# Performance work log

Measured on AMD Instinct MI355X. Metric: run time of the kernel, lower is better.

## Reference

```python
import jax, jax.numpy as jnp
import numpy as np

DIM = 128
N_GNN = 3
VDW_N = 6.0
MAX_VDW = 0.0356
MIN_VDW = 0.0178
DEV_VDW_RADIUS = 0.2
DM_MIN = 0.5


def gated_gat(x, adj, W, Wb, A, gW, gb):
    # PIGNet-style GatedGAT: attention from bilinear form, gated residual
    h = x @ W + Wb                                   # [B,N,D]
    e = jnp.einsum('bjl,bkl->bjk', h @ A, h)
    e = e + jnp.swapaxes(e, 1, 2)
    att = jnp.where(adj > 0, e, -9e15)
    att = jax.nn.softmax(att, axis=-1) * adj
    hp = jax.nn.relu(jnp.einsum('bij,bjd->bid', att, h))
    coeff = jax.nn.sigmoid(jnp.concatenate([x, hp], axis=-1) @ gW + gb)  # [B,N,1]
    return coeff * x + (1.0 - coeff) * hp


def pair_mlp(lig, tgt, W1, b1, W2, b2):
    # MLP on concat([lig_i, tgt_j]) without materializing [B,L,T,2D]:
    # split W1 along its input dim (exact same math as concat @ W1)
    D = lig.shape[-1]
    pre = (jnp.einsum('bld,dk->blk', lig, W1[:D])[:, :, None, :]
           + jnp.einsum('btd,dk->btk', tgt, W1[D:])[:, None, :, :] + b1)
    h = jax.nn.relu(pre)                             # [B,L,T,D]
    return jnp.einsum('bltk,ko->blt', h, W2) + b2[0]  # [B,L,T]


def setup_inputs() -> dict:
    key = jax.random.key(0)
    ks = jax.random.split(key, 20)
    B, L, T, D = 8, 128, 512, DIM
    f32 = jnp.float32

    def adj(k, n, p):
        a = (jax.random.uniform(k, (B, n, n)) < p).astype(f32)
        a = jnp.maximum(a, jnp.swapaxes(a, 1, 2))
        return jnp.minimum(a + jnp.eye(n, dtype=f32), 1.0)

    s = 0.05
    inp = dict(
        ligand_h=jax.random.normal(ks[0], (B, L, 54), f32),
        target_h=jax.random.normal(ks[1], (B, T, 54), f32),
        ligand_adj=adj(ks[2], L, 0.10),
        target_adj=adj(ks[3], T, 0.02),
        interaction_indice=(jax.random.uniform(ks[4], (B, 3, L, T)) < 0.05).astype(f32),
        ligand_pos=jax.random.uniform(ks[5], (B, L, 3), f32) * 20.0,
        target_pos=jax.random.uniform(ks[6], (B, T, 3), f32) * 20.0,
        rotor=jnp.floor(jax.random.uniform(ks[7], (B, 1), f32) * 10.0),
        ligand_vdw_radii=jax.random.uniform(ks[8], (B, L), f32) * 0.5 + 1.5,
        target_vdw_radii=jax.random.uniform(ks[9], (B, T), f32) * 0.5 + 1.5,
        ligand_valid=jnp.ones((B, L), f32),
        target_valid=jnp.ones((B, T), f32),
        emb_W=jax.random.normal(ks[10], (54, D), f32) * s,
        gat_W=jax.random.normal(ks[11], (N_GNN, D, D), f32) * s,
        gat_Wb=jnp.zeros((N_GNN, D), f32),
        gat_A=jax.random.normal(ks[12], (N_GNN, D, D), f32) * s,
        gat_gW=jax.random.normal(ks[13], (N_GNN, 2 * D, 1), f32) * s,
        gat_gb=jnp.zeros((N_GNN, 1), f32),
        vdwA_W1=jax.random.normal(ks[14], (2 * D, D), f32) * s,
        vdwA_b1=jnp.zeros((D,), f32),
        vdwA_W2=jax.random.normal(ks[15], (D, 1), f32) * s,
        vdwA_b2=jnp.zeros((1,), f32),
        dc_W1=jax.random.normal(ks[16], (2 * D, D), f32) * s,
        dc_b1=jnp.zeros((D,), f32),
        dc_W2=jax.random.normal(ks[17], (D, 1), f32) * s,
        dc_b2=jnp.zeros((1,), f32),
        hbond_coeff=jnp.array([1.0], f32),
        metal_coeff=jnp.array([1.0], f32),
        hydrophobic_coeff=jnp.array([0.5], f32),
        rotor_coeff=jnp.array([0.5], f32),
    )
    return inp


def reference(ligand_h, target_h, ligand_adj, target_adj, interaction_indice,
              ligand_pos, target_pos, rotor, ligand_vdw_radii, target_vdw_radii,
              ligand_valid, target_valid, emb_W, gat_W, gat_Wb, gat_A, gat_gW,
              gat_gb, vdwA_W1, vdwA_b1, vdwA_W2, vdwA_b2, dc_W1, dc_b1, dc_W2,
              dc_b2, hbond_coeff, metal_coeff, hydrophobic_coeff, rotor_coeff):
    lig = ligand_h @ emb_W
    tgt = target_h @ emb_W
    # pairwise distance matrix with min-distance clamp
    diff = ligand_pos[:, :, None, :] - target_pos[:, None, :, :]
    dm = jnp.sqrt((diff * diff).sum(-1) + 1e-10)      # [B,L,T]
    dm = jnp.where(dm < DM_MIN, 1e10, dm)
    for i in range(N_GNN):  # eval mode: dropout is identity
        lig = gated_gat(lig, ligand_adj, gat_W[i], gat_Wb[i], gat_A[i], gat_gW[i], gat_gb[i])
        tgt = gated_gat(tgt, target_adj, gat_W[i], gat_Wb[i], gat_A[i], gat_gW[i], gat_gb[i])
    vdws_sum = ligand_vdw_radii[:, :, None] + target_vdw_radii[:, None, :]
    # dm_correction=True: tanh MLP on pairwise concat features, scaled by dev_vdw_radius
    vdws_sum = vdws_sum + jnp.tanh(pair_mlp(lig, tgt, dc_W1, dc_b1, dc_W2, dc_b2)) * DEV_VDW_RADIUS
    # --- vdw term ---
    dm_0 = jnp.where(vdws_sum < 1e-4, 1.0, vdws_sum)
    ratio = dm_0 / dm
    valid = ligand_valid[:, :, None] * target_valid[:, None, :]
    energy = jnp.minimum(ratio ** (2.0 * VDW_N) - 2.0 * ratio ** VDW_N, 100.0) * valid
    A = jax.nn.sigmoid(pair_mlp(lig, tgt, vdwA_W1, vdwA_b1, vdwA_W2, vdwA_b2))
    A = A * (MAX_VDW - MIN_VDW) + MIN_VDW
    vdw_e = (A * energy).sum((1, 2))                  # [B]
    # --- hbond / metal / hydrophobic ramps share dm - vdws_sum ---
    d = dm - vdws_sum
    ramp = jnp.clip(d / -0.7, 0.0, 1.0)
    hbond_e = -(hbond_coeff[0] ** 2) * (ramp * interaction_indice[:, 0]).sum((1, 2))
    metal_e = -(metal_coeff[0] ** 2) * (ramp * interaction_indice[:, 1]).sum((1, 2))
    ramp2 = jnp.clip(-d + 1.5, 0.0, 1.0)
    hydro_e = -(hydrophobic_coeff[0] ** 2) * (ramp2 * interaction_indice[:, 2]).sum((1, 2))
    energies = jnp.stack([vdw_e, hbond_e, metal_e, hydro_e], axis=-1)  # [B,4]
    energies = energies / (1.0 + rotor_coeff[0] ** 2 * rotor)          # rotor penalty
    return energies
```

## Files before the change

### kernel.cpp

```cpp
#include <hip/hip_runtime.h>
#include <hip/hip_bf16.h>
#include <math.h>

typedef __hip_bfloat16 bf16;

#define DIMD 128
#define BB 8
#define LL 128
#define TT 512

#define BMT 64
#define BKT 32
#define TGT_TILES 36
#define LIG_TILES 3

#define CV_EMBW   0L
#define CV_GATW   (CV_EMBW + 54 * 128)
#define CV_GATA   (CV_GATW + 3 * 128 * 128)
#define CV_WB     (CV_GATA + 3 * 128 * 128)
#define CV_DCW1   (CV_WB + 3 * 128)
#define CV_VW1    (CV_DCW1 + 2 * 128 * 128)
#define CV_TOTAL  (CV_VW1 + 2 * 128 * 128)

__device__ __forceinline__ float LD(const void* p, long i, int bf) {
    if (bf) return __bfloat162float(((const bf16*)p)[i]);
    return ((const float*)p)[i];
}

__global__ void init_ws(const unsigned int* __restrict__ embw_raw,
                        float* __restrict__ accum, int* __restrict__ flagp) {
    int t = threadIdx.x;
    if (t < 32) accum[t] = 0.0f;
    if (t == 0) {
        int cnt = 0;
        for (int k = 0; k < 256; ++k) {
            unsigned int b = (embw_raw[k] >> 8) & 0xffu;
            unsigned int e = b & 0x7fu;
            if (e >= 0x38u && e <= 0x3fu) ++cnt;
        }
        *flagp = (cnt > 128) ? 1 : 0;
    }
}

__global__ void cvt_weights(const void* __restrict__ embW, const void* __restrict__ gatW,
                            const void* __restrict__ gatA, const void* __restrict__ gatWb,
                            const void* __restrict__ dcW1, const void* __restrict__ vW1,
                            float* __restrict__ out, const int* __restrict__ flagp) {
    int bf = *flagp;
    long i = (long)blockIdx.x * 256 + threadIdx.x;
    if (i >= CV_TOTAL) return;
    float v;
    if (i < CV_GATW)      v = LD(embW, i - CV_EMBW, bf);
    else if (i < CV_GATA) v = LD(gatW, i - CV_GATW, bf);
    else if (i < CV_WB)   v = LD(gatA, i - CV_GATA, bf);
    else if (i < CV_DCW1) v = LD(gatWb, i - CV_WB, bf);
    else if (i < CV_VW1)  v = LD(dcW1, i - CV_DCW1, bf);
    else                  v = LD(vW1, i - CV_VW1, bf);
    out[i] = v;
}

__global__ void embed_both(const void* __restrict__ Xl, const void* __restrict__ Xt,
                           const float* __restrict__ Wf, float* __restrict__ out,
                           int K, const int* __restrict__ flagp) {
    __shared__ float xrow[DIMD];
    int bf = *flagp;
    int row = blockIdx.x;
    int d = threadIdx.x;
    const void* X; long r;
    if (row < BB * LL) { X = Xl; r = row; }
    else               { X = Xt; r = row - BB * LL; }
    if (d < K) xrow[d] = LD(X, r * K + d, bf);
    __syncthreads();
    float acc = 0.0f;
    for (int k = 0; k < K; ++k)
        acc = fmaf(xrow[k], Wf[(long)k * DIMD + d], acc);
    out[(long)row * DIMD + d] = acc;
}

__global__ void gemm_hha4(const float* __restrict__ X, const float* __restrict__ Wf,
                          const float* __restrict__ Af, const float* __restrict__ Wbf,
                          int layer, float* __restrict__ hout, float* __restrict__ hAout) {
    __shared__ float xs[4][DIMD];
    __shared__ float hs[4][DIMD];
    long row0 = (long)blockIdx.x * 4;
    int d = threadIdx.x & 127, rg = threadIdx.x >> 7;
    xs[rg * 2 + 0][d] = X[(row0 + rg * 2 + 0) * DIMD + d];
    xs[rg * 2 + 1][d] = X[(row0 + rg * 2 + 1) * DIMD + d];
    __syncthreads();
    const float* W = Wf + (long)layer * DIMD * DIMD;
    const float* A = Af + (long)layer * DIMD * DIMD;
    float b = Wbf[layer * DIMD + d];
    float h0 = b, h1 = b;
    const float* x0 = xs[rg * 2];
    const float* x1 = xs[rg * 2 + 1];
#pragma unroll 8
    for (int k = 0; k < DIMD; ++k) {
        float w = W[(long)k * DIMD + d];
        h0 = fmaf(x0[k], w, h0);
        h1 = fmaf(x1[k], w, h1);
    }
    long ob = (row0 + rg * 2) * DIMD + d;
    hout[ob] = h0; hout[ob + DIMD] = h1;
    hs[rg * 2][d] = h0; hs[rg * 2 + 1][d] = h1;
    __syncthreads();
    float a0 = 0.0f, a1 = 0.0f;
    const float* g0 = hs[rg * 2];
    const float* g1 = hs[rg * 2 + 1];
#pragma unroll 8
    for (int k = 0; k < DIMD; ++k) {
        float w = A[(long)k * DIMD + d];
        a0 = fmaf(g0[k], w, a0);
        a1 = fmaf(g1[k], w, a1);
    }
    hAout[ob] = a0;
    hAout[ob + DIMD] = a1;
}

__global__ void esym_both(const float* __restrict__ hA_t, const float* __restrict__ h_t,
                          float* __restrict__ e_t,
                          const float* __restrict__ hA_l, const float* __restrict__ h_l,
                          float* __restrict__ e_l) {
    __shared__ float At[BKT][BMT + 4];
    __shared__ float Bt[BKT][BMT + 4];
    int idx = blockIdx.x, b = blockIdx.y, t = threadIdx.x;
    const float *hA, *h; float* e; int N;
    if (idx < TGT_TILES) { hA = hA_t; h = h_t; e = e_t; N = TT; }
    else { idx -= TGT_TILES; hA = hA_l; h = h_l; e = e_l; N = LL; }
    int jt = (int)((sqrtf(8.0f * idx + 1.0f) - 1.0f) * 0.5f);
    while ((jt + 1) * (jt + 2) / 2 <= idx) ++jt;
    while (jt * (jt + 1) / 2 > idx) --jt;
    int kt = idx - jt * (jt + 1) / 2;
    const float* hAb = hA + (long)b * N * DIMD;
    const float* hb  = h  + (long)b * N * DIMD;
    int tm = t & 15, tn = t >> 4;
    int k4 = (t & 7) * 4;
    int row0 = t >> 3;
    float acc[4][4];
#pragma unroll
    for (int i = 0; i < 4; ++i)
#pragma unroll
        for (int jj = 0; jj < 4; ++jj) acc[i][jj] = 0.0f;

#pragma unroll
    for (int c = 0; c < 8; ++c) {
        const float* Ap = (c < 4) ? hAb : hb;
        const float* Bp = (c < 4) ? hb : hAb;
        int ko = (c & 3) * BKT;
        __syncthreads();
#pragma unroll
        for (int rr = 0; rr < 2; ++rr) {
            int row = row0 + rr * 32;
            float4 av = *(const float4*)&Ap[(long)(jt * BMT + row) * DIMD + ko + k4];
            float4 bv = *(const float4*)&Bp[(long)(kt * BMT + row) * DIMD + ko + k4];
            At[k4 + 0][row] = av.x; At[k4 + 1][row] = av.y;
            At[k4 + 2][row] = av.z; At[k4 + 3][row] = av.w;
            Bt[k4 + 0][row] = bv.x; Bt[k4 + 1][row] = bv.y;
            Bt[k4 + 2][row] = bv.z; Bt[k4 + 3][row] = bv.w;
        }
        __syncthreads();
#pragma unroll
        for (int k = 0; k < BKT; ++k) {
            float4 a4 = *(const float4*)&At[k][tm * 4];
            float4 b4 = *(const float4*)&Bt[k][tn * 4];
            float A[4] = {a4.x, a4.y, a4.z, a4.w};
            float Bv[4] = {b4.x, b4.y, b4.z, b4.w};
#pragma unroll
            for (int i = 0; i < 4; ++i)
#pragma unroll
                for (int jj = 0; jj < 4; ++jj)
                    acc[i][jj] = fmaf(A[i], Bv[jj], acc[i][jj]);
        }
    }
    long ebN = (long)b * N;
    long ebase = (ebN + jt * BMT + tm * 4) * N + kt * BMT + tn * 4;
#pragma unroll
    for (int i = 0; i < 4; ++i) {
        float4 v;
        v.x = acc[i][0]; v.y = acc[i][1]; v.z = acc[i][2]; v.w = acc[i][3];
        *(float4*)&e[ebase + (long)i * N] = v;
    }
    if (jt != kt) {
        long mbase = (ebN + kt * BMT + tn * 4) * N + jt * BMT + tm * 4;
#pragma unroll
        for (int jj = 0; jj < 4; ++jj) {
            float4 v;
            v.x = acc[0][jj]; v.y = acc[1][jj]; v.z = acc[2][jj]; v.w = acc[3][jj];
            *(float4*)&e[mbase + (long)jj * N] = v;
        }
    }
}

template<int CNT>
__device__ __forceinline__ void softmax_row(float* __restrict__ erow,
                                            const void* __restrict__ adj,
                                            long adjbase, int bf) {
    int lane = threadIdx.x & 63;
    float vals[CNT], av[CNT];
    float m = -3.4e38f;
#pragma unroll
    for (int i = 0; i < CNT; ++i) {
        int k = lane + i * 64;
        float a = LD(adj, adjbase + k, bf);
        float v = (a > 0.0f) ? erow[k] : -9e15f;
        av[i] = a; vals[i] = v;
        m = fmaxf(m, v);
    }
#pragma unroll
    for (int s = 32; s > 0; s >>= 1) m = fmaxf(m, __shfl_xor(m, s));
    float sum = 0.0f;
#pragma unroll
    for (int i = 0; i < CNT; ++i) { vals[i] = expf(vals[i] - m); sum += vals[i]; }
#pragma unroll
    for (int s = 32; s > 0; s >>= 1) sum += __shfl_xor(sum, s);
    float inv = 1.0f / sum;
#pragma unroll
    for (int i = 0; i < CNT; ++i)
        erow[lane + i * 64] = vals[i] * av[i] * inv;
}

__global__ void att_softmax_both(float* __restrict__ e_t, float* __restrict__ e_l,
                                 const void* __restrict__ adj_t, const void* __restrict__ adj_l,
                                 const int* __restrict__ flagp) {
    int bf = *flagp;
    int b = blockIdx.y, x = blockIdx.x;
    int jr = threadIdx.x >> 6;
    if (x < TT / 4) {
        int j = x * 4 + jr;
        long base = ((long)b * TT + j) * TT;
        softmax_row<8>(e_t + base, adj_t, base, bf);
    } else {
        int j = (x - TT / 4) * 4 + jr;
        long base = ((long)b * LL + j) * LL;
        softmax_row<2>(e_l + base, adj_l, base, bf);
    }
}

__global__ void hp_gemm_both(const float* __restrict__ att_t, const float* __restrict__ h_t,
                             float* __restrict__ p0_t, float* __restrict__ p1_t,
                             const float* __restrict__ att_l, const float* __restrict__ h_l,
                             float* __restrict__ p0_l, float* __restrict__ p1_l) {
    __shared__ float At[32][36];
    __shared__ float Ht[32][DIMD];
    int jt = blockIdx.x, kc = blockIdx.y, b = blockIdx.z;
    int t = threadIdx.x;
    const float *att, *h; float *part0, *part1; int N;
    if (jt < 16) { att = att_t; h = h_t; part0 = p0_t; part1 = p1_t; N = TT; }
    else { jt -= 16; att = att_l; h = h_l; part0 = p0_l; part1 = p1_l; N = LL; }
    const float* attb = att + (long)b * N * N;
    const float* hb = h + (long)b * N * DIMD;
    int tm = t & 7, tn = t >> 3;
    float acc[4][4] = {};
    int kchunk = N / 2;
    int kbeg = kc * kchunk;
    int ar = t >> 3;
    int ac4 = (t & 7) * 4;
    int hk = t >> 5;
    int hc4 = (t & 31) * 4;
    for (int k0 = kbeg; k0 < kbeg + kchunk; k0 += 32) {
        __syncthreads();
        float4 av = *(const float4*)&attb[(long)(jt * 32 + ar) * N + k0 + ac4];
        At[ac4 + 0][ar] = av.x; At[ac4 + 1][ar] = av.y;
        At[ac4 + 2][ar] = av.z; At[ac4 + 3][ar] = av.w;
#pragma unroll
        for (int p = 0; p < 4; ++p)
            *(float4*)&Ht[hk + p * 8][hc4] = *(const float4*)&hb[(long)(k0 + hk + p * 8) * DIMD + hc4];
        __syncthreads();
#pragma unroll
        for (int k = 0; k < 32; ++k) {
            float4 a4 = *(const float4*)&At[k][tm * 4];
            float4 h4 = *(const float4*)&Ht[k][tn * 4];
            float A[4] = {a4.x, a4.y, a4.z, a4.w};
            float H[4] = {h4.x, h4.y, h4.z, h4.w};
#pragma unroll
            for (int i = 0; i < 4; ++i)
#pragma unroll
                for (int jj = 0; jj < 4; ++jj)
                    acc[i][jj] = fmaf(A[i], H[jj], acc[i][jj]);
        }
    }
    float* outp = (kc == 0) ? part0 : part1;
    long obase = ((long)b * N + jt * 32 + tm * 4) * DIMD + tn * 4;
#pragma unroll
    for (int i = 0; i < 4; ++i) {
        float4 v; v.x = acc[i][0]; v.y = acc[i][1]; v.z = acc[i][2]; v.w = acc[i][3];
        *(float4*)&outp[obase + (long)i * DIMD] = v;
    }
}

__global__ void gat_gate_both(float* __restrict__ x_t, float* __restrict__ x_l,
                              const float* __restrict__ p0_t, const float* __restrict__ p1_t,
                              const float* __restrict__ p0_l, const float* __restrict__ p1_l,
                              const void* __restrict__ gW, long offgW,
                              const void* __restrict__ gb, long offgb,
                              const int* __restrict__ flagp) {
    int bf = *flagp;
    int b = blockIdx.y, x = blockIdx.x;
    int jr = threadIdx.x >> 6, lane = threadIdx.x & 63;
    float* xb; const float *part0, *part1; long rbase;
    if (x < TT / 4) {
        int j = x * 4 + jr;
        rbase = ((long)b * TT + j) * DIMD;
        xb = x_t; part0 = p0_t; part1 = p1_t;
    } else {
        int j = (x - TT / 4) * 4 + jr;
        rbase = ((long)b * LL + j) * DIMD;
        xb = x_l; part0 = p0_l; part1 = p1_l;
    }
    float* xrow = xb + rbase;
    float hp0 = fmaxf(part0[rbase + lane] + part1[rbase + lane], 0.0f);
    float hp1 = fmaxf(part0[rbase + lane + 64] + part1[rbase + lane + 64], 0.0f);
    float x0 = xrow[lane], x1 = xrow[lane + 64];
    float g = x0 * LD(gW, offgW + lane, bf) + x1 * LD(gW, offgW + lane + 64, bf)
            + hp0 * LD(gW, offgW + DIMD + lane, bf) + hp1 * LD(gW, offgW + DIMD + lane + 64, bf);
#pragma unroll
    for (int s = 32; s > 0; s >>= 1) g += __shfl_xor(g, s);
    g += LD(gb, offgb, bf);
    float coeff = 1.0f / (1.0f + expf(-g));
    xrow[lane] = coeff * x0 + (1.0f - coeff) * hp0;
    xrow[lane + 64] = coeff * x1 + (1.0f - coeff) * hp1;
}

__global__ void proj_both4(const float* __restrict__ X,
                           const float* __restrict__ Wdcf, const void* __restrict__ bdc,
                           const float* __restrict__ WAf, const void* __restrict__ bA,
                           long rowsplit, float* __restrict__ outdc, float* __restrict__ outA,
                           const int* __restrict__ flagp) {
    __shared__ float xs[4][DIMD];
    int bf = *flagp;
    const float* Wf; const void* bias; float* out;
    if (blockIdx.y == 0) { Wf = Wdcf; bias = bdc; out = outdc; }
    else                 { Wf = WAf;  bias = bA;  out = outA; }
    long row0 = (long)blockIdx.x * 4;
    int d = threadIdx.x & 127, rg = threadIdx.x >> 7;
    int sideb = row0 >= rowsplit;
    const float* W = Wf + (sideb ? (long)DIMD * DIMD : 0);
    xs[rg * 2 + 0][d] = X[(row0 + rg * 2 + 0) * DIMD + d];
    xs[rg * 2 + 1][d] = X[(row0 + rg * 2 + 1) * DIMD + d];
    __syncthreads();
    float b0 = sideb ? 0.0f : LD(bias, d, bf);
    float a0 = b0, a1 = b0;
    const float* x0 = xs[rg * 2];
    const float* x1 = xs[rg * 2 + 1];
#pragma unroll 8
    for (int k = 0; k < DIMD; ++k) {
        float w = W[(long)k * DIMD + d];
        a0 = fmaf(x0[k], w, a0);
        a1 = fmaf(x1[k], w, a1);
    }
    long ob = (row0 + rg * 2) * DIMD + d;
    out[ob] = a0;
    out[ob + DIMD] = a1;
}

__global__ void transpose_both(const float* __restrict__ in0, float* __restrict__ out0,
                               const float* __restrict__ in1, float* __restrict__ out1) {
    __shared__ float tile[32][33];
    int z = blockIdx.z;
    const float* in; float* outT; int b;
    if (z < BB) { in = in0; outT = out0; b = z; }
    else        { in = in1; outT = out1; b = z - BB; }
    int n0 = blockIdx.x * 32;
    int d0 = blockIdx.y * 32;
    int t = threadIdx.x;
    int tx = t & 31, ty = t >> 5;
    for (int r = ty; r < 32; r += 8)
        tile[r][tx] = in[((long)b * TT + n0 + r) * DIMD + d0 + tx];
    __syncthreads();
    for (int r = ty; r < 32; r += 8)
        outT[((long)b * DIMD + d0 + r) * TT + n0 + tx] = tile[tx][r];
}

__global__ void pair_energy(const float* __restrict__ ligdc, const float* __restrict__ tgtdcT,
                            const float* __restrict__ ligA, const float* __restrict__ tgtAT,
                            const void* __restrict__ dcW2, const void* __restrict__ dcb2,
                            const void* __restrict__ AW2, const void* __restrict__ Ab2,
                            const void* __restrict__ lpos, const void* __restrict__ tpos,
                            const void* __restrict__ lrad, const void* __restrict__ trad,
                            const void* __restrict__ lval, const void* __restrict__ tval,
                            const void* __restrict__ ii, float* __restrict__ accum,
                            const int* __restrict__ flagp) {
    int bf = *flagp;
    int l0 = blockIdx.x * 2, b = blockIdx.y, t = threadIdx.x;
    __shared__ __align__(16) float sdc0[DIMD], sdc1[DIMD], sA0[DIMD], sA1[DIMD];
    __shared__ __align__(16) float w2dc[DIMD], w2A[DIMD];
    __shared__ float red[256];
    if (t < DIMD) {
        sdc0[t] = ligdc[((long)b * LL + l0) * DIMD + t];
        sA0[t]  = ligA [((long)b * LL + l0) * DIMD + t];
        w2dc[t] = LD(dcW2, t, bf);
        w2A[t]  = LD(AW2, t, bf);
    } else {
        int u = t - DIMD;
        sdc1[u] = ligdc[((long)b * LL + l0 + 1) * DIMD + u];
        sA1[u]  = ligA [((long)b * LL + l0 + 1) * DIMD + u];
    }
    __syncthreads();
    int tt0 = t * 2;
    const float* tdT = tgtdcT + (long)b * DIMD * TT;
    const float* taT = tgtAT  + (long)b * DIMD * TT;
    float adc00 = 0.0f, adc01 = 0.0f, adc10 = 0.0f, adc11 = 0.0f;
    float aA00 = 0.0f, aA01 = 0.0f, aA10 = 0.0f, aA11 = 0.0f;
    for (int i4 = 0; i4 < DIMD; i4 += 4) {
        float4 wd = *(const float4*)&w2dc[i4];
        float4 wa = *(const float4*)&w2A[i4];
        float4 v0d = *(const float4*)&sdc0[i4];
        float4 v1d = *(const float4*)&sdc1[i4];
        float4 v0a = *(const float4*)&sA0[i4];
        float4 v1a = *(const float4*)&sA1[i4];
        float wdv[4] = {wd.x, wd.y, wd.z, wd.w};
        float wav[4] = {wa.x, wa.y, wa.z, wa.w};
        float s0d[4] = {v0d.x, v0d.y, v0d.z, v0d.w};
        float s1d[4] = {v1d.x, v1d.y, v1d.z, v1d.w};
        float s0a[4] = {v0a.x, v0a.y, v0a.z, v0a.w};
        float s1a[4] = {v1a.x, v1a.y, v1a.z, v1a.w};
#pragma unroll
        for (int j = 0; j < 4; ++j) {
            float2 td = *(const float2*)&tdT[(long)(i4 + j) * TT + tt0];
            float2 ta = *(const float2*)&taT[(long)(i4 + j) * TT + tt0];
            adc00 = fmaf(fmaxf(td.x + s0d[j], 0.0f), wdv[j], adc00);
            adc01 = fmaf(fmaxf(td.y + s0d[j], 0.0f), wdv[j], adc01);
            adc10 = fmaf(fmaxf(td.x + s1d[j], 0.0f), wdv[j], adc10);
            adc11 = fmaf(fmaxf(td.y + s1d[j], 0.0f), wdv[j], adc11);
            aA00 = fmaf(fmaxf(ta.x + s0a[j], 0.0f), wav[j], aA00);
            aA01 = fmaf(fmaxf(ta.y + s0a[j], 0.0f), wav[j], aA01);
            aA10 = fmaf(fmaxf(ta.x + s1a[j], 0.0f), wav[j], aA10);
            aA11 = fmaf(fmaxf(ta.y + s1a[j], 0.0f), wav[j], aA11);
        }
    }
    float lx0 = LD(lpos, ((long)b * LL + l0) * 3 + 0, bf);
    float ly0 = LD(lpos, ((long)b * LL + l0) * 3 + 1, bf);
    float lz0 = LD(lpos, ((long)b * LL + l0) * 3 + 2, bf);
    float lx1 = LD(lpos, ((long)b * LL + l0 + 1) * 3 + 0, bf);
    float ly1 = LD(lpos, ((long)b * LL + l0 + 1) * 3 + 1, bf);
    float lz1 = LD(lpos, ((long)b * LL + l0 + 1) * 3 + 2, bf);
    float lr0 = LD(lrad, (long)b * LL + l0, bf);
    float lr1 = LD(lrad, (long)b * LL + l0 + 1, bf);
    float lv0 = LD(lval, (long)b * LL + l0, bf);
    float lv1 = LD(lval, (long)b * LL + l0 + 1, bf);
    float cdcb2 = LD(dcb2, 0, bf), cab2 = LD(Ab2, 0, bf);
    long iiA0 = ((long)(b * 3 + 0) * LL + l0) * TT;
    long iiB0 = ((long)(b * 3 + 1) * LL + l0) * TT;
    long iiC0 = ((long)(b * 3 + 2) * LL + l0) * TT;
    long iiA1 = iiA0 + TT, iiB1 = iiB0 + TT, iiC1 = iiC0 + TT;
    float p0 = 0.0f, p1 = 0.0f, p2 = 0.0f, p3 = 0.0f;
#pragma unroll
    for (int jj = 0; jj < 2; ++jj) {
        int tt = tt0 + jj;
        float tx = LD(tpos, ((long)b * TT + tt) * 3 + 0, bf);
        float ty = LD(tpos, ((long)b * TT + tt) * 3 + 1, bf);
        float tz = LD(tpos, ((long)b * TT + tt) * 3 + 2, bf);
        float tr = LD(trad, (long)b * TT + tt, bf);
        float tv = LD(tval, (long)b * TT + tt, bf);
#pragma unroll
        for (int li = 0; li < 2; ++li) {
            float dx = (li ? lx1 : lx0) - tx;
            float dy = (li ? ly1 : ly0) - ty;
            float dz = (li ? lz1 : lz0) - tz;
            float dm = sqrtf(dx * dx + dy * dy + dz * dz + 1e-10f);
            if (dm < 0.5f) dm = 1e10f;
            float adcv = jj ? (li ? adc11 : adc01) : (li ? adc10 : adc00);
            float aAv  = jj ? (li ? aA11  : aA01)  : (li ? aA10  : aA00);
            float dev = tanhf(adcv + cdcb2) * 0.2f;
            float vdws = (li ? lr1 : lr0) + tr + dev;
            float dm0 = (vdws < 1e-4f) ? 1.0f : vdws;
            float ratio = dm0 / dm;
            float r2 = ratio * ratio, r6 = r2 * r2 * r2, r12 = r6 * r6;
            float en = fminf(r12 - 2.0f * r6, 100.0f) * (li ? lv1 : lv0) * tv;
            float As = 1.0f / (1.0f + expf(-(aAv + cab2)));
            As = As * (0.0356f - 0.0178f) + 0.0178f;
            p0 = fmaf(As, en, p0);
            float dd = dm - vdws;
            float ramp = fminf(fmaxf(dd * (1.0f / -0.7f), 0.0f), 1.0f);
            p1 = fmaf(ramp, LD(ii, (li ? iiA1 : iiA0) + tt, bf), p1);
            p2 = fmaf(ramp, LD(ii, (li ? iiB1 : iiB0) + tt, bf), p2);
            float ramp2 = fminf(fmaxf(-dd + 1.5f, 0.0f), 1.0f);
            p3 = fmaf(ramp2, LD(ii, (li ? iiC1 : iiC0) + tt, bf), p3);
        }
    }
    for (int e = 0; e < 4; ++e) {
        float v = (e == 0) ? p0 : (e == 1) ? p1 : (e == 2) ? p2 : p3;
        red[t] = v; __syncthreads();
        for (int s = 128; s > 0; s >>= 1) { if (t < s) red[t] += red[t + s]; __syncthreads(); }
        if (t == 0) atomicAdd(&accum[b * 4 + e], red[0]);
        __syncthreads();
    }
}

__global__ void finalize(const float* __restrict__ accum, const void* __restrict__ hb,
                         const void* __restrict__ mc, const void* __restrict__ hyd,
                         const void* __restrict__ rc, const void* __restrict__ rotor,
                         void* __restrict__ out, const int* __restrict__ flagp) {
    int bf = *flagp;
    int t = threadIdx.x;
    if (t >= 32) return;
    int b = t >> 2, e = t & 3;
    float v = accum[t];
    if (e == 1) { float c = LD(hb, 0, bf);  v = -c * c * v; }
    else if (e == 2) { float c = LD(mc, 0, bf);  v = -c * c * v; }
    else if (e == 3) { float c = LD(hyd, 0, bf); v = -c * c * v; }
    float r = LD(rc, 0, bf);
    float den = 1.0f + r * r * LD(rotor, b, bf);
    float res = v / den;
    if (bf) ((bf16*)out)[t] = __float2bfloat16(res);
    else    ((float*)out)[t] = res;
}

extern "C" void kernel_launch(void* const* d_in, const int* in_sizes, int n_in,
                              void* d_out, int out_size, void* d_ws, size_t ws_size,
                              hipStream_t stream) {
    const void* ligand_h = d_in[0];
    const void* target_h = d_in[1];
    const void* ligand_adj = d_in[2];
    const void* target_adj = d_in[3];
    const void* interaction_indice = d_in[4];
    const void* ligand_pos = d_in[5];
    const void* target_pos = d_in[6];
    const void* rotor = d_in[7];
    const void* ligand_vdw = d_in[8];
    const void* target_vdw = d_in[9];
    const void* ligand_valid = d_in[10];
    const void* target_valid = d_in[11];
    const void* emb_W = d_in[12];
    const void* gat_W = d_in[13];
    const void* gat_Wb = d_in[14];
    const void* gat_A = d_in[15];
    const void* gat_gW = d_in[16];
    const void* gat_gb = d_in[17];
    const void* vdwA_W1 = d_in[18];
    const void* vdwA_b1 = d_in[19];
    const void* vdwA_W2 = d_in[20];
    const void* vdwA_b2 = d_in[21];
    const void* dc_W1 = d_in[22];
    const void* dc_b1 = d_in[23];
    const void* dc_W2 = d_in[24];
    const void* dc_b2 = d_in[25];
    const void* hbond_coeff = d_in[26];
    const void* metal_coeff = d_in[27];
    const void* hydrophobic_coeff = d_in[28];
    const void* rotor_coeff = d_in[29];

    float* ws = (float*)d_ws;
    size_t off = 0;
    float* lig_x = ws + off;  off += (size_t)BB * LL * DIMD;
    float* tgt_x = ws + off;  off += (size_t)BB * TT * DIMD;
    float* h_lig = ws + off;  off += (size_t)BB * LL * DIMD;
    float* h_tgt = ws + off;  off += (size_t)BB * TT * DIMD;
    float* hA_lig = ws + off; off += (size_t)BB * LL * DIMD;
    float* hA_tgt = ws + off; off += (size_t)BB * TT * DIMD;
    float* accum = ws + off;  off += 32;
    int* flagp = (int*)(ws + off); off += 2;
    float* e_buf = ws + off;  off += (size_t)BB * TT * TT;
    float* e_lig = ws + off;  off += (size_t)BB * LL * LL;
    float* part1 = ws + off;  off += (size_t)BB * (TT + LL) * DIMD;
    float* cvw   = ws + off;  off += (size_t)CV_TOTAL;
    float* part1_t = part1;
    float* part1_l = part1 + (size_t)BB * TT * DIMD;
    float* part0_lig = hA_lig;
    float* part0_tgt = hA_tgt;
    float* ligdc = h_lig;
    float* ligA = hA_lig;
    float* tgtdc = h_tgt;
    float* tgtA  = hA_tgt;
    float* tgtdcT = e_buf;
    float* tgtAT  = e_buf + (size_t)BB * DIMD * TT;
    float* wEmb = cvw + CV_EMBW;
    float* wGat = cvw + CV_GATW;
    float* wGatA = cvw + CV_GATA;
    float* wWb  = cvw + CV_WB;
    float* wDc1 = cvw + CV_DCW1;
    float* wV1  = cvw + CV_VW1;

    init_ws<<<1, 64, 0, stream>>>((const unsigned int*)emb_W, accum, flagp);
    cvt_weights<<<(CV_TOTAL + 255) / 256, 256, 0, stream>>>(
        emb_W, gat_W, gat_A, gat_Wb, dc_W1, vdwA_W1, cvw, flagp);

    embed_both<<<BB * (LL + TT), DIMD, 0, stream>>>(ligand_h, target_h, wEmb, lig_x, 54, flagp);

    const long ROWSPLIT = (long)BB * LL;
    for (int i = 0; i < 3; ++i) {
        long offgW = (long)i * 2 * DIMD;
        long offgb = i;
        gemm_hha4<<<BB * (LL + TT) / 4, 256, 0, stream>>>(
            lig_x, wGat, wGatA, wWb, i, h_lig, hA_lig);
        esym_both<<<dim3(TGT_TILES + LIG_TILES, BB), 256, 0, stream>>>(
            hA_tgt, h_tgt, e_buf, hA_lig, h_lig, e_lig);
        att_softmax_both<<<dim3(TT / 4 + LL / 4, BB), 256, 0, stream>>>(
            e_buf, e_lig, target_adj, ligand_adj, flagp);
        hp_gemm_both<<<dim3(20, 2, BB), 256, 0, stream>>>(
            e_buf, h_tgt, part0_tgt, part1_t, e_lig, h_lig, part0_lig, part1_l);
        gat_gate_both<<<dim3(TT / 4 + LL / 4, BB), 256, 0, stream>>>(
            tgt_x, lig_x, part0_tgt, part1_t, part0_lig, part1_l,
            gat_gW, offgW, gat_gb, offgb, flagp);
    }

    proj_both4<<<dim3(BB * (LL + TT) / 4, 2), 256, 0, stream>>>(
        lig_x, wDc1, dc_b1, wV1, vdwA_b1, ROWSPLIT, ligdc, ligA, flagp);

    transpose_both<<<dim3(TT / 32, DIMD / 32, 2 * BB), 256, 0, stream>>>(
        tgtdc, tgtdcT, tgtA, tgtAT);

    pair_energy<<<dim3(LL / 2, BB), 256, 0, stream>>>(
        ligdc, tgtdcT, ligA, tgtAT, dc_W2, dc_b2, vdwA_W2, vdwA_b2,
        ligand_pos, target_pos, ligand_vdw, target_vdw,
        ligand_valid, target_valid, interaction_indice, accum, flagp);

    finalize<<<1, 64, 0, stream>>>(accum, hbond_coeff, metal_coeff,
                                   hydrophobic_coeff, rotor_coeff, rotor, d_out, flagp);
}
```

Before: 391.5 us.

## Fuse gating into next GEMM, split esym halves, merge init kernels, widen pair grid

Merges the flag-detection and weight-conversion kernels into one launch, and folds the GAT gate step into the next layer's h/hA GEMM or the final projection kernel, so three launches and one pass over x are removed. The symmetric attention-score GEMM is split into two independent halves written to separate buffers and summed inside softmax. This doubles the block count but adds an extra N×N buffer read. The pair-energy kernel now uses one target per thread with twice as many blocks, raising parallelism at the cost of less register reuse. The gate is recomputed redundantly in both y-blocks of proj_gate.

```diff
diff --git a/kernel.cpp b/kernel.cpp
--- a/kernel.cpp
+++ b/kernel.cpp
@@ -18,7 +18,9 @@
 #define CV_GATW   (CV_EMBW + 54 * 128)
 #define CV_GATA   (CV_GATW + 3 * 128 * 128)
 #define CV_WB     (CV_GATA + 3 * 128 * 128)
-#define CV_DCW1   (CV_WB + 3 * 128)
+#define CV_GGW    (CV_WB + 3 * 128)
+#define CV_GGB    (CV_GGW + 3 * 2 * 128)
+#define CV_DCW1   (CV_GGB + 4)
 #define CV_VW1    (CV_DCW1 + 2 * 128 * 128)
 #define CV_TOTAL  (CV_VW1 + 2 * 128 * 128)
 
@@ -27,33 +29,35 @@
     return ((const float*)p)[i];
 }
 
-__global__ void init_ws(const unsigned int* __restrict__ embw_raw,
-                        float* __restrict__ accum, int* __restrict__ flagp) {
+__global__ void init_cvt(const unsigned int* __restrict__ embw_raw,
+                         const void* __restrict__ embW, const void* __restrict__ gatW,
+                         const void* __restrict__ gatA, const void* __restrict__ gatWb,
+                         const void* __restrict__ ggW, const void* __restrict__ ggb,
+                         const void* __restrict__ dcW1, const void* __restrict__ vW1,
+                         float* __restrict__ out, float* __restrict__ accum,
+                         int* __restrict__ flagp) {
+    __shared__ int cnts;
     int t = threadIdx.x;
-    if (t < 32) accum[t] = 0.0f;
-    if (t == 0) {
-        int cnt = 0;
-        for (int k = 0; k < 256; ++k) {
-            unsigned int b = (embw_raw[k] >> 8) & 0xffu;
-            unsigned int e = b & 0x7fu;
-            if (e >= 0x38u && e <= 0x3fu) ++cnt;
-        }
-        *flagp = (cnt > 128) ? 1 : 0;
-    }
-}
-
-__global__ void cvt_weights(const void* __restrict__ embW, const void* __restrict__ gatW,
-                            const void* __restrict__ gatA, const void* __restrict__ gatWb,
-                            const void* __restrict__ dcW1, const void* __restrict__ vW1,
-                            float* __restrict__ out, const int* __restrict__ flagp) {
-    int bf = *flagp;
-    long i = (long)blockIdx.x * 256 + threadIdx.x;
+    if (t == 0) cnts = 0;
+    __syncthreads();
+    unsigned int bword = (embw_raw[t] >> 8) & 0xffu;
+    unsigned int e = bword & 0x7fu;
+    if (e >= 0x38u && e <= 0x3fu) atomicAdd(&cnts, 1);
+    __syncthreads();
+    int bf = cnts > 128;
+    if (blockIdx.x == 0) {
+        if (t < 32) accum[t] = 0.0f;
+        if (t == 0) *flagp = bf;
+    }
+    long i = (long)blockIdx.x * 256 + t;
     if (i >= CV_TOTAL) return;
     float v;
-    if (i < CV_GATW)      v = LD(embW, i - CV_EMBW, bf);
+    if (i < CV_GATW)      v = LD(embW, i, bf);
     else if (i < CV_GATA) v = LD(gatW, i - CV_GATW, bf);
     else if (i < CV_WB)   v = LD(gatA, i - CV_GATA, bf);
-    else if (i < CV_DCW1) v = LD(gatWb, i - CV_WB, bf);
+    else if (i < CV_GGW)  v = LD(gatWb, i - CV_WB, bf);
+    else if (i < CV_GGB)  v = LD(ggW, i - CV_GGW, bf);
+    else if (i < CV_DCW1) { long j = i - CV_GGB; v = (j < 3) ? LD(ggb, j, bf) : 0.0f; }
     else if (i < CV_VW1)  v = LD(dcW1, i - CV_DCW1, bf);
     else                  v = LD(vW1, i - CV_VW1, bf);
     out[i] = v;
@@ -77,61 +81,89 @@
     out[(long)row * DIMD + d] = acc;
 }
 
-__global__ void gemm_hha4(const float* __restrict__ X, const float* __restrict__ Wf,
-                          const float* __restrict__ Af, const float* __restrict__ Wbf,
-                          int layer, float* __restrict__ hout, float* __restrict__ hAout) {
+__global__ void gemm_hha_gate(float* __restrict__ X, const float* __restrict__ P0,
+                              const float* __restrict__ P1, const float* __restrict__ cvw,
+                              int layer, int dogate,
+                              float* __restrict__ hout, float* __restrict__ hAout) {
     __shared__ float xs[4][DIMD];
     __shared__ float hs[4][DIMD];
+    __shared__ float gred[4][2];
     long row0 = (long)blockIdx.x * 4;
     int d = threadIdx.x & 127, rg = threadIdx.x >> 7;
-    xs[rg * 2 + 0][d] = X[(row0 + rg * 2 + 0) * DIMD + d];
-    xs[rg * 2 + 1][d] = X[(row0 + rg * 2 + 1) * DIMD + d];
-    __syncthreads();
-    const float* W = Wf + (long)layer * DIMD * DIMD;
-    const float* A = Af + (long)layer * DIMD * DIMD;
-    float b = Wbf[layer * DIMD + d];
+    int w = threadIdx.x >> 6, lane = threadIdx.x & 63;
+    long r0 = row0 + rg * 2, r1 = r0 + 1;
+    float xv0 = X[r0 * DIMD + d];
+    float xv1 = X[r1 * DIMD + d];
+    if (dogate) {
+        const float* gW = cvw + CV_GGW + (long)(layer - 1) * 2 * DIMD;
+        float gb = cvw[CV_GGB + (layer - 1)];
+        float hp0 = fmaxf(P0[r0 * DIMD + d] + P1[r0 * DIMD + d], 0.0f);
+        float hp1 = fmaxf(P0[r1 * DIMD + d] + P1[r1 * DIMD + d], 0.0f);
+        float s0 = xv0 * gW[d] + hp0 * gW[DIMD + d];
+        float s1 = xv1 * gW[d] + hp1 * gW[DIMD + d];
+#pragma unroll
+        for (int s = 32; s > 0; s >>= 1) { s0 += __shfl_xor(s0, s); s1 += __shfl_xor(s1, s); }
+        if (lane == 0) { gred[rg * 2 + 0][w & 1] = s0; gred[rg * 2 + 1][w & 1] = s1; }
+        __syncthreads();
+        float g0 = gred[rg * 2 + 0][0] + gred[rg * 2 + 0][1] + gb;
+        float g1 = gred[rg * 2 + 1][0] + gred[rg * 2 + 1][1] + gb;
+        float c0 = 1.0f / (1.0f + expf(-g0));
+        float c1 = 1.0f / (1.0f + expf(-g1));
+        xv0 = c0 * xv0 + (1.0f - c0) * hp0;
+        xv1 = c1 * xv1 + (1.0f - c1) * hp1;
+        X[r0 * DIMD + d] = xv0;
+        X[r1 * DIMD + d] = xv1;
+    }
+    xs[rg * 2 + 0][d] = xv0;
+    xs[rg * 2 + 1][d] = xv1;
+    __syncthreads();
+    const float* W = cvw + CV_GATW + (long)layer * DIMD * DIMD;
+    const float* A = cvw + CV_GATA + (long)layer * DIMD * DIMD;
+    float b = cvw[CV_WB + layer * DIMD + d];
     float h0 = b, h1 = b;
     const float* x0 = xs[rg * 2];
     const float* x1 = xs[rg * 2 + 1];
 #pragma unroll 8
     for (int k = 0; k < DIMD; ++k) {
-        float w = W[(long)k * DIMD + d];
-        h0 = fmaf(x0[k], w, h0);
-        h1 = fmaf(x1[k], w, h1);
-    }
-    long ob = (row0 + rg * 2) * DIMD + d;
+        float wv = W[(long)k * DIMD + d];
+        h0 = fmaf(x0[k], wv, h0);
+        h1 = fmaf(x1[k], wv, h1);
+    }
+    long ob = r0 * DIMD + d;
     hout[ob] = h0; hout[ob + DIMD] = h1;
     hs[rg * 2][d] = h0; hs[rg * 2 + 1][d] = h1;
     __syncthreads();
     float a0 = 0.0f, a1 = 0.0f;
-    const float* g0 = hs[rg * 2];
-    const float* g1 = hs[rg * 2 + 1];
+    const float* g0p = hs[rg * 2];
+    const float* g1p = hs[rg * 2 + 1];
 #pragma unroll 8
     for (int k = 0; k < DIMD; ++k) {
-        float w = A[(long)k * DIMD + d];
-        a0 = fmaf(g0[k], w, a0);
-        a1 = fmaf(g1[k], w, a1);
+        float wv = A[(long)k * DIMD + d];
+        a0 = fmaf(g0p[k], wv, a0);
+        a1 = fmaf(g1p[k], wv, a1);
     }
     hAout[ob] = a0;
     hAout[ob + DIMD] = a1;
 }
 
 __global__ void esym_both(const float* __restrict__ hA_t, const float* __restrict__ h_t,
-                          float* __restrict__ e_t,
+                          float* __restrict__ e1_t, float* __restrict__ e2_t,
                           const float* __restrict__ hA_l, const float* __restrict__ h_l,
-                          float* __restrict__ e_l) {
+                          float* __restrict__ e1_l, float* __restrict__ e2_l) {
     __shared__ float At[BKT][BMT + 4];
     __shared__ float Bt[BKT][BMT + 4];
-    int idx = blockIdx.x, b = blockIdx.y, t = threadIdx.x;
+    int idx = blockIdx.x, half = blockIdx.y, b = blockIdx.z, t = threadIdx.x;
     const float *hA, *h; float* e; int N;
-    if (idx < TGT_TILES) { hA = hA_t; h = h_t; e = e_t; N = TT; }
-    else { idx -= TGT_TILES; hA = hA_l; h = h_l; e = e_l; N = LL; }
+    if (idx < TGT_TILES) { hA = hA_t; h = h_t; e = half ? e2_t : e1_t; N = TT; }
+    else { idx -= TGT_TILES; hA = hA_l; h = h_l; e = half ? e2_l : e1_l; N = LL; }
     int jt = (int)((sqrtf(8.0f * idx + 1.0f) - 1.0f) * 0.5f);
     while ((jt + 1) * (jt + 2) / 2 <= idx) ++jt;
     while (jt * (jt + 1) / 2 > idx) --jt;
     int kt = idx - jt * (jt + 1) / 2;
     const float* hAb = hA + (long)b * N * DIMD;
     const float* hb  = h  + (long)b * N * DIMD;
+    const float* Ap = half ? hb : hAb;
+    const float* Bp = half ? hAb : hb;
     int tm = t & 15, tn = t >> 4;
     int k4 = (t & 7) * 4;
     int row0 = t >> 3;
@@ -142,10 +174,8 @@
         for (int jj = 0; jj < 4; ++jj) acc[i][jj] = 0.0f;
 
 #pragma unroll
-    for (int c = 0; c < 8; ++c) {
-        const float* Ap = (c < 4) ? hAb : hb;
-        const float* Bp = (c < 4) ? hb : hAb;
-        int ko = (c & 3) * BKT;
+    for (int c = 0; c < 4; ++c) {
+        int ko = c * BKT;
         __syncthreads();
 #pragma unroll
         for (int rr = 0; rr < 2; ++rr) {
@@ -191,7 +221,8 @@
 }
 
 template<int CNT>
-__device__ __forceinline__ void softmax_row(float* __restrict__ erow,
+__device__ __forceinline__ void softmax_row(float* __restrict__ e1row,
+                                            const float* __restrict__ e2row,
                                             const void* __restrict__ adj,
                                             long adjbase, int bf) {
     int lane = threadIdx.x & 63;
@@ -201,7 +232,7 @@
     for (int i = 0; i < CNT; ++i) {
         int k = lane + i * 64;
         float a = LD(adj, adjbase + k, bf);
-        float v = (a > 0.0f) ? erow[k] : -9e15f;
+        float v = (a > 0.0f) ? (e1row[k] + e2row[k]) : -9e15f;
         av[i] = a; vals[i] = v;
         m = fmaxf(m, v);
     }
@@ -215,10 +246,11 @@
     float inv = 1.0f / sum;
 #pragma unroll
     for (int i = 0; i < CNT; ++i)
-        erow[lane + i * 64] = vals[i] * av[i] * inv;
-}
-
-__global__ void att_softmax_both(float* __restrict__ e_t, float* __restrict__ e_l,
+        e1row[lane + i * 64] = vals[i] * av[i] * inv;
+}
+
+__global__ void att_softmax_both(float* __restrict__ e1_t, const float* __restrict__ e2_t,
+                                 float* __restrict__ e1_l, const float* __restrict__ e2_l,
                                  const void* __restrict__ adj_t, const void* __restrict__ adj_l,
                                  const int* __restrict__ flagp) {
     int bf = *flagp;
@@ -227,11 +259,11 @@
     if (x < TT / 4) {
         int j = x * 4 + jr;
         long base = ((long)b * TT + j) * TT;
-        softmax_row<8>(e_t + base, adj_t, base, bf);
+        softmax_row<8>(e1_t + base, e2_t + base, adj_t, base, bf);
     } else {
         int j = (x - TT / 4) * 4 + jr;
         long base = ((long)b * LL + j) * LL;
-        softmax_row<2>(e_l + base, adj_l, base, bf);
+        softmax_row<2>(e1_l + base, e2_l + base, adj_l, base, bf);
     }
 }
 
@@ -287,67 +319,57 @@
     }
 }
 
-__global__ void gat_gate_both(float* __restrict__ x_t, float* __restrict__ x_l,
-                              const float* __restrict__ p0_t, const float* __restrict__ p1_t,
-                              const float* __restrict__ p0_l, const float* __restrict__ p1_l,
-                              const void* __restrict__ gW, long offgW,
-                              const void* __restrict__ gb, long offgb,
-                              const int* __restrict__ flagp) {
+__global__ void proj_gate(const float* __restrict__ X, const float* __restrict__ P0,
+                          const float* __restrict__ P1, const float* __restrict__ cvw,
+                          const void* __restrict__ bdc, const void* __restrict__ bA,
+                          long rowsplit, float* __restrict__ outdc, float* __restrict__ outA,
+                          const int* __restrict__ flagp) {
+    __shared__ float xs[4][DIMD];
+    __shared__ float gred[4][2];
     int bf = *flagp;
-    int b = blockIdx.y, x = blockIdx.x;
-    int jr = threadIdx.x >> 6, lane = threadIdx.x & 63;
-    float* xb; const float *part0, *part1; long rbase;
-    if (x < TT / 4) {
-        int j = x * 4 + jr;
-        rbase = ((long)b * TT + j) * DIMD;
-        xb = x_t; part0 = p0_t; part1 = p1_t;
-    } else {
-        int j = (x - TT / 4) * 4 + jr;
-        rbase = ((long)b * LL + j) * DIMD;
-        xb = x_l; part0 = p0_l; part1 = p1_l;
-    }
-    float* xrow = xb + rbase;
-    float hp0 = fmaxf(part0[rbase + lane] + part1[rbase + lane], 0.0f);
-    float hp1 = fmaxf(part0[rbase + lane + 64] + part1[rbase + lane + 64], 0.0f);
-    float x0 = xrow[lane], x1 = xrow[lane + 64];
-    float g = x0 * LD(gW, offgW + lane, bf) + x1 * LD(gW, offgW + lane + 64, bf)
-            + hp0 * LD(gW, offgW + DIMD + lane, bf) + hp1 * LD(gW, offgW + DIMD + lane + 64, bf);
-#pragma unroll
-    for (int s = 32; s > 0; s >>= 1) g += __shfl_xor(g, s);
-    g += LD(gb, offgb, bf);
-    float coeff = 1.0f / (1.0f + expf(-g));
-    xrow[lane] = coeff * x0 + (1.0f - coeff) * hp0;
-    xrow[lane + 64] = coeff * x1 + (1.0f - coeff) * hp1;
-}
-
-__global__ void proj_both4(const float* __restrict__ X,
-                           const float* __restrict__ Wdcf, const void* __restrict__ bdc,
-                           const float* __restrict__ WAf, const void* __restrict__ bA,
-                           long rowsplit, float* __restrict__ outdc, float* __restrict__ outA,
-                           const int* __restrict__ flagp) {
-    __shared__ float xs[4][DIMD];
-    int bf = *flagp;
-    const float* Wf; const void* bias; float* out;
-    if (blockIdx.y == 0) { Wf = Wdcf; bias = bdc; out = outdc; }
-    else                 { Wf = WAf;  bias = bA;  out = outA; }
     long row0 = (long)blockIdx.x * 4;
     int d = threadIdx.x & 127, rg = threadIdx.x >> 7;
+    int w = threadIdx.x >> 6, lane = threadIdx.x & 63;
+    long r0 = row0 + rg * 2, r1 = r0 + 1;
+    float xv0 = X[r0 * DIMD + d];
+    float xv1 = X[r1 * DIMD + d];
+    {
+        const float* gW = cvw + CV_GGW + 2L * 2 * DIMD;
+        float gb = cvw[CV_GGB + 2];
+        float hp0 = fmaxf(P0[r0 * DIMD + d] + P1[r0 * DIMD + d], 0.0f);
+        float hp1 = fmaxf(P0[r1 * DIMD + d] + P1[r1 * DIMD + d], 0.0f);
+        float s0 = xv0 * gW[d] + hp0 * gW[DIMD + d];
+        float s1 = xv1 * gW[d] + hp1 * gW[DIMD + d];
+#pragma unroll
+        for (int s = 32; s > 0; s >>= 1) { s0 += __shfl_xor(s0, s); s1 += __shfl_xor(s1, s); }
+        if (lane == 0) { gred[rg * 2 + 0][w & 1] = s0; gred[rg * 2 + 1][w & 1] = s1; }
+        __syncthreads();
+        float g0 = gred[rg * 2 + 0][0] + gred[rg * 2 + 0][1] + gb;
+        float g1 = gred[rg * 2 + 1][0] + gred[rg * 2 + 1][1] + gb;
+        float c0 = 1.0f / (1.0f + expf(-g0));
+        float c1 = 1.0f / (1.0f + expf(-g1));
+        xv0 = c0 * xv0 + (1.0f - c0) * hp0;
+        xv1 = c1 * xv1 + (1.0f - c1) * hp1;
+    }
+    xs[rg * 2 + 0][d] = xv0;
+    xs[rg * 2 + 1][d] = xv1;
+    __syncthreads();
+    const float* Wf = (blockIdx.y == 0) ? (cvw + CV_DCW1) : (cvw + CV_VW1);
+    const void* bias = (blockIdx.y == 0) ? bdc : bA;
+    float* out = (blockIdx.y == 0) ? outdc : outA;
     int sideb = row0 >= rowsplit;
     const float* W = Wf + (sideb ? (long)DIMD * DIMD : 0);
-    xs[rg * 2 + 0][d] = X[(row0 + rg * 2 + 0) * DIMD + d];
-    xs[rg * 2 + 1][d] = X[(row0 + rg * 2 + 1) * DIMD + d];
-    __syncthreads();
     float b0 = sideb ? 0.0f : LD(bias, d, bf);
     float a0 = b0, a1 = b0;
     const float* x0 = xs[rg * 2];
     const float* x1 = xs[rg * 2 + 1];
 #pragma unroll 8
     for (int k = 0; k < DIMD; ++k) {
-        float w = W[(long)k * DIMD + d];
-        a0 = fmaf(x0[k], w, a0);
-        a1 = fmaf(x1[k], w, a1);
-    }
-    long ob = (row0 + rg * 2) * DIMD + d;
+        float wv = W[(long)k * DIMD + d];
+        a0 = fmaf(x0[k], wv, a0);
+        a1 = fmaf(x1[k], wv, a1);
+    }
+    long ob = r0 * DIMD + d;
     out[ob] = a0;
     out[ob + DIMD] = a1;
 }
@@ -380,7 +402,8 @@
                             const void* __restrict__ ii, float* __restrict__ accum,
                             const int* __restrict__ flagp) {
     int bf = *flagp;
-    int l0 = blockIdx.x * 2, b = blockIdx.y, t = threadIdx.x;
+    int l0 = blockIdx.x * 2, b = blockIdx.z, t = threadIdx.x;
+    int tt = blockIdx.y * 256 + t;
     __shared__ __align__(16) float sdc0[DIMD], sdc1[DIMD], sA0[DIMD], sA1[DIMD];
     __shared__ __align__(16) float w2dc[DIMD], w2A[DIMD];
     __shared__ float red[256];
@@ -395,36 +418,19 @@
         sA1[u]  = ligA [((long)b * LL + l0 + 1) * DIMD + u];
     }
     __syncthreads();
-    int tt0 = t * 2;
     const float* tdT = tgtdcT + (long)b * DIMD * TT;
     const float* taT = tgtAT  + (long)b * DIMD * TT;
-    float adc00 = 0.0f, adc01 = 0.0f, adc10 = 0.0f, adc11 = 0.0f;
-    float aA00 = 0.0f, aA01 = 0.0f, aA10 = 0.0f, aA11 = 0.0f;
+    float adc0 = 0.0f, adc1 = 0.0f, aA0 = 0.0f, aA1 = 0.0f;
     for (int i4 = 0; i4 < DIMD; i4 += 4) {
-        float4 wd = *(const float4*)&w2dc[i4];
-        float4 wa = *(const float4*)&w2A[i4];
-        float4 v0d = *(const float4*)&sdc0[i4];
-        float4 v1d = *(const float4*)&sdc1[i4];
-        float4 v0a = *(const float4*)&sA0[i4];
-        float4 v1a = *(const float4*)&sA1[i4];
-        float wdv[4] = {wd.x, wd.y, wd.z, wd.w};
-        float wav[4] = {wa.x, wa.y, wa.z, wa.w};
-        float s0d[4] = {v0d.x, v0d.y, v0d.z, v0d.w};
-        float s1d[4] = {v1d.x, v1d.y, v1d.z, v1d.w};
-        float s0a[4] = {v0a.x, v0a.y, v0a.z, v0a.w};
-        float s1a[4] = {v1a.x, v1a.y, v1a.z, v1a.w};
 #pragma unroll
         for (int j = 0; j < 4; ++j) {
-            float2 td = *(const float2*)&tdT[(long)(i4 + j) * TT + tt0];
-            float2 ta = *(const float2*)&taT[(long)(i4 + j) * TT + tt0];
-            adc00 = fmaf(fmaxf(td.x + s0d[j], 0.0f), wdv[j], adc00);
-            adc01 = fmaf(fmaxf(td.y + s0d[j], 0.0f), wdv[j], adc01);
-            adc10 = fmaf(fmaxf(td.x + s1d[j], 0.0f), wdv[j], adc10);
-            adc11 = fmaf(fmaxf(td.y + s1d[j], 0.0f), wdv[j], adc11);
-            aA00 = fmaf(fmaxf(ta.x + s0a[j], 0.0f), wav[j], aA00);
-            aA01 = fmaf(fmaxf(ta.y + s0a[j], 0.0f), wav[j], aA01);
-            aA10 = fmaf(fmaxf(ta.x + s1a[j], 0.0f), wav[j], aA10);
-            aA11 = fmaf(fmaxf(ta.y + s1a[j], 0.0f), wav[j], aA11);
+            float td = tdT[(long)(i4 + j) * TT + tt];
+            float ta = taT[(long)(i4 + j) * TT + tt];
+            float wd = w2dc[i4 + j], wa = w2A[i4 + j];
+            adc0 = fmaf(fmaxf(td + sdc0[i4 + j], 0.0f), wd, adc0);
+            adc1 = fmaf(fmaxf(td + sdc1[i4 + j], 0.0f), wd, adc1);
+            aA0  = fmaf(fmaxf(ta + sA0[i4 + j],  0.0f), wa, aA0);
+            aA1  = fmaf(fmaxf(ta + sA1[i4 + j],  0.0f), wa, aA1);
         }
     }
     float lx0 = LD(lpos, ((long)b * LL + l0) * 3 + 0, bf);
@@ -442,40 +448,36 @@
     long iiB0 = ((long)(b * 3 + 1) * LL + l0) * TT;
     long iiC0 = ((long)(b * 3 + 2) * LL + l0) * TT;
     long iiA1 = iiA0 + TT, iiB1 = iiB0 + TT, iiC1 = iiC0 + TT;
+    float tx = LD(tpos, ((long)b * TT + tt) * 3 + 0, bf);
+    float ty = LD(tpos, ((long)b * TT + tt) * 3 + 1, bf);
+    float tz = LD(tpos, ((long)b * TT + tt) * 3 + 2, bf);
+    float tr = LD(trad, (long)b * TT + tt, bf);
+    float tv = LD(tval, (long)b * TT + tt, bf);
     float p0 = 0.0f, p1 = 0.0f, p2 = 0.0f, p3 = 0.0f;
 #pragma unroll
-    for (int jj = 0; jj < 2; ++jj) {
-        int tt = tt0 + jj;
-        float tx = LD(tpos, ((long)b * TT + tt) * 3 + 0, bf);
-        float ty = LD(tpos, ((long)b * TT + tt) * 3 + 1, bf);
-        float tz = LD(tpos, ((long)b * TT + tt) * 3 + 2, bf);
-        float tr = LD(trad, (long)b * TT + tt, bf);
-        float tv = LD(tval, (long)b * TT + tt, bf);
-#pragma unroll
-        for (int li = 0; li < 2; ++li) {
-            float dx = (li ? lx1 : lx0) - tx;
-            float dy = (li ? ly1 : ly0) - ty;
-            float dz = (li ? lz1 : lz0) - tz;
-            float dm = sqrtf(dx * dx + dy * dy + dz * dz + 1e-10f);
-            if (dm < 0.5f) dm = 1e10f;
-            float adcv = jj ? (li ? adc11 : adc01) : (li ? adc10 : adc00);
-            float aAv  = jj ? (li ? aA11  : aA01)  : (li ? aA10  : aA00);
-            float dev = tanhf(adcv + cdcb2) * 0.2f;
-            float vdws = (li ? lr1 : lr0) + tr + dev;
-            float dm0 = (vdws < 1e-4f) ? 1.0f : vdws;
-            float ratio = dm0 / dm;
-            float r2 = ratio * ratio, r6 = r2 * r2 * r2, r12 = r6 * r6;
-            float en = fminf(r12 - 2.0f * r6, 100.0f) * (li ? lv1 : lv0) * tv;
-            float As = 1.0f / (1.0f + expf(-(aAv + cab2)));
-            As = As * (0.0356f - 0.0178f) + 0.0178f;
-            p0 = fmaf(As, en, p0);
-            float dd = dm - vdws;
-            float ramp = fminf(fmaxf(dd * (1.0f / -0.7f), 0.0f), 1.0f);
-            p1 = fmaf(ramp, LD(ii, (li ? iiA1 : iiA0) + tt, bf), p1);
-            p2 = fmaf(ramp, LD(ii, (li ? iiB1 : iiB0) + tt, bf), p2);
-            float ramp2 = fminf(fmaxf(-dd + 1.5f, 0.0f), 1.0f);
-            p3 = fmaf(ramp2, LD(ii, (li ? iiC1 : iiC0) + tt, bf), p3);
-        }
+    for (int li = 0; li < 2; ++li) {
+        float dx = (li ? lx1 : lx0) - tx;
+        float dy = (li ? ly1 : ly0) - ty;
+        float dz = (li ? lz1 : lz0) - tz;
+        float dm = sqrtf(dx * dx + dy * dy + dz * dz + 1e-10f);
+        if (dm < 0.5f) dm = 1e10f;
+        float adcv = li ? adc1 : adc0;
+        float aAv  = li ? aA1  : aA0;
+        float dev = tanhf(adcv + cdcb2) * 0.2f;
+        float vdws = (li ? lr1 : lr0) + tr + dev;
+        float dm0 = (vdws < 1e-4f) ? 1.0f : vdws;
+        float ratio = dm0 / dm;
+        float r2 = ratio * ratio, r6 = r2 * r2 * r2, r12 = r6 * r6;
+        float en = fminf(r12 - 2.0f * r6, 100.0f) * (li ? lv1 : lv0) * tv;
+        float As = 1.0f / (1.0f + expf(-(aAv + cab2)));
+        As = As * (0.0356f - 0.0178f) + 0.0178f;
+        p0 = fmaf(As, en, p0);
+        float dd = dm - vdws;
+        float ramp = fminf(fmaxf(dd * (1.0f / -0.7f), 0.0f), 1.0f);
+        p1 = fmaf(ramp, LD(ii, (li ? iiA1 : iiA0) + tt, bf), p1);
+        p2 = fmaf(ramp, LD(ii, (li ? iiB1 : iiB0) + tt, bf), p2);
+        float ramp2 = fminf(fmaxf(-dd + 1.5f, 0.0f), 1.0f);
+        p3 = fmaf(ramp2, LD(ii, (li ? iiC1 : iiC0) + tt, bf), p3);
     }
     for (int e = 0; e < 4; ++e) {
         float v = (e == 0) ? p0 : (e == 1) ? p1 : (e == 2) ? p2 : p3;
@@ -551,55 +553,48 @@
     int* flagp = (int*)(ws + off); off += 2;
     float* e_buf = ws + off;  off += (size_t)BB * TT * TT;
     float* e_lig = ws + off;  off += (size_t)BB * LL * LL;
-    float* part1 = ws + off;  off += (size_t)BB * (TT + LL) * DIMD;
+    float* e2_buf = ws + off; off += (size_t)BB * TT * TT;
+    float* e2_lig = ws + off; off += (size_t)BB * LL * LL;
+    float* part1 = ws + off;  off += (size_t)BB * (LL + TT) * DIMD;
+    float* projA = ws + off;  off += (size_t)BB * (LL + TT) * DIMD;
     float* cvw   = ws + off;  off += (size_t)CV_TOTAL;
-    float* part1_t = part1;
-    float* part1_l = part1 + (size_t)BB * TT * DIMD;
+    float* part1_l = part1;
+    float* part1_t = part1 + (size_t)BB * LL * DIMD;
     float* part0_lig = hA_lig;
     float* part0_tgt = hA_tgt;
     float* ligdc = h_lig;
-    float* ligA = hA_lig;
     float* tgtdc = h_tgt;
-    float* tgtA  = hA_tgt;
+    float* ligA = projA;
+    float* tgtA = projA + (size_t)BB * LL * DIMD;
     float* tgtdcT = e_buf;
     float* tgtAT  = e_buf + (size_t)BB * DIMD * TT;
     float* wEmb = cvw + CV_EMBW;
-    float* wGat = cvw + CV_GATW;
-    float* wGatA = cvw + CV_GATA;
-    float* wWb  = cvw + CV_WB;
-    float* wDc1 = cvw + CV_DCW1;
-    float* wV1  = cvw + CV_VW1;
-
-    init_ws<<<1, 64, 0, stream>>>((const unsigned int*)emb_W, accum, flagp);
-    cvt_weights<<<(CV_TOTAL + 255) / 256, 256, 0, stream>>>(
-        emb_W, gat_W, gat_A, gat_Wb, dc_W1, vdwA_W1, cvw, flagp);
+
+    init_cvt<<<(CV_TOTAL + 255) / 256, 256, 0, stream>>>(
+        (const unsigned int*)emb_W, emb_W, gat_W, gat_A, gat_Wb,
+        gat_gW, gat_gb, dc_W1, vdwA_W1, cvw, accum, flagp);
 
     embed_both<<<BB * (LL + TT), DIMD, 0, stream>>>(ligand_h, target_h, wEmb, lig_x, 54, flagp);
 
     const long ROWSPLIT = (long)BB * LL;
     for (int i = 0; i < 3; ++i) {
-        long offgW = (long)i * 2 * DIMD;
-        long offgb = i;
-        gemm_hha4<<<BB * (LL + TT) / 4, 256, 0, stream>>>(
-            lig_x, wGat, wGatA, wWb, i, h_lig, hA_lig);
-        esym_both<<<dim3(TGT_TILES + LIG_TILES, BB), 256, 0, stream>>>(
-            hA_tgt, h_tgt, e_buf, hA_lig, h_lig, e_lig);
+        gemm_hha_gate<<<BB * (LL + TT) / 4, 256, 0, stream>>>(
+            lig_x, hA_lig, part1, cvw, i, i > 0 ? 1 : 0, h_lig, hA_lig);
+        esym_both<<<dim3(TGT_TILES + LIG_TILES, 2, BB), 256, 0, stream>>>(
+            hA_tgt, h_tgt, e_buf, e2_buf, hA_lig, h_lig, e_lig, e2_lig);
         att_softmax_both<<<dim3(TT / 4 + LL / 4, BB), 256, 0, stream>>>(
-            e_buf, e_lig, target_adj, ligand_adj, flagp);
+            e_buf, e2_buf, e_lig, e2_lig, target_adj, ligand_adj, flagp);
         hp_gemm_both<<<dim3(20, 2, BB), 256, 0, stream>>>(
             e_buf, h_tgt, part0_tgt, part1_t, e_lig, h_lig, part0_lig, part1_l);
-        gat_gate_both<<<dim3(TT / 4 + LL / 4, BB), 256, 0, stream>>>(
-            tgt_x, lig_x, part0_tgt, part1_t, part0_lig, part1_l,
-            gat_gW, offgW, gat_gb, offgb, flagp);
-    }
-
-    proj_both4<<<dim3(BB * (LL + TT) / 4, 2), 256, 0, stream>>>(
-        lig_x, wDc1, dc_b1, wV1, vdwA_b1, ROWSPLIT, ligdc, ligA, flagp);
+    }
+
+    proj_gate<<<dim3(BB * (LL + TT) / 4, 2), 256, 0, stream>>>(
+        lig_x, hA_lig, part1, cvw, dc_b1, vdwA_b1, ROWSPLIT, ligdc, ligA, flagp);
 
     transpose_both<<<dim3(TT / 32, DIMD / 32, 2 * BB), 256, 0, stream>>>(
         tgtdc, tgtdcT, tgtA, tgtAT);
 
-    pair_energy<<<dim3(LL / 2, BB), 256, 0, stream>>>(
+    pair_energy<<<dim3(LL / 2, 2, BB), 256, 0, stream>>>(
         ligdc, tgtdcT, ligA, tgtAT, dc_W2, dc_b2, vdwA_W2, vdwA_b2,
         ligand_pos, target_pos, ligand_vdw, target_vdw,
         ligand_valid, target_valid, interaction_indice, accum, flagp);
```

New measurement: 384.4 us. About the same (-1.8%).
